# Performance work log

Measured on AMD Instinct MI355X. Metric: run time of the kernel, lower is better.

## Reference

```python
import jax, jax.numpy as jnp
import numpy as np

SIZE = 4096
LOG_N = 12  # log2(SIZE)
BATCH = 8192


def setup_inputs() -> dict:
    key = jax.random.key(0)
    k1, k2 = jax.random.split(key)
    x = jax.random.normal(k1, (BATCH, SIZE), dtype=jnp.float32)
    # one (SIZE//2, 2, 2) real twiddle bank per layer, stacked; init ~ randn/sqrt(2)
    twiddles = jax.random.normal(k2, (LOG_N, SIZE // 2, 2, 2), dtype=jnp.float32) / np.sqrt(2.0).astype(np.float32)
    return {"x": x, "twiddles": twiddles}


def _butterfly_forward(x, twiddles):
    # x: [B, n]; twiddles: [log_n, n//2, 2, 2]
    B, n = x.shape
    log_n = twiddles.shape[0]
    out = x
    for layer in range(log_n):
        stride = 2 ** (log_n - layer - 1)
        n_blocks = n // (2 * stride)
        # block b, offset i: top = out[:, b, 0, i], bot = out[:, b, 1, i]
        xr = out.reshape(B, n_blocks, 2, stride)
        top = xr[:, :, 0, :]  # [B, nb, stride]
        bot = xr[:, :, 1, :]
        # twiddle_idx = b*stride + i  ->  reshape to (nb, stride, 2, 2)
        w = twiddles[layer].reshape(n_blocks, stride, 2, 2)
        new_top = w[None, :, :, 0, 0] * top + w[None, :, :, 0, 1] * bot
        new_bot = w[None, :, :, 1, 0] * top + w[None, :, :, 1, 1] * bot
        out = jnp.stack([new_top, new_bot], axis=2).reshape(B, n)
    return out


def reference(x, twiddles):
    return _butterfly_forward(x, twiddles)
```

## Files before the change

kernel.cpp:

```cpp
#include <hip/hip_runtime.h>

#define ROWS 4
#define N 4096
#define BATCH 8192
#define S_AB 264
#define HALF 5248
#define S_BC 328
#define NWS_F4 (8 * 2048)

typedef float v4f __attribute__((ext_vector_type(4)));

__device__ __forceinline__ void layer_compute(float (&v)[ROWS][16],
                                              const float4 (&w)[8],
                                              const int bit) {
    const int d = 1 << bit;
    #pragma unroll
    for (int pc = 0; pc < 8; ++pc) {
        const int lo = ((pc >> bit) << (bit + 1)) | (pc & (d - 1));
        const int hi = lo + d;
        #pragma unroll
        for (int r = 0; r < ROWS; ++r) {
            const float top = v[r][lo];
            const float bot = v[r][hi];
            v[r][lo] = w[pc].x * top + w[pc].y * bot;
            v[r][hi] = w[pc].z * top + w[pc].w * bot;
        }
    }
}

__global__ __launch_bounds__(256)
void permute_tw_kernel(const float* __restrict__ tw, float4* __restrict__ nws) {
    const int i = blockIdx.x * 256 + threadIdx.x;
    const int s  = i >> 11;
    const int j  = i & 2047;
    const int pc = j >> 8;
    const int a  = (j >> 4) & 15;
    const int cb = j & 15;
    const float4* tw4 = (const float4*)tw;
    const int src = (s < 4) ? (a * 128 + pc * 16 + cb)
                            : (a * 128 + cb * 8 + pc);
    nws[i] = tw4[(4 + s) * 2048 + src];
}

__global__ __launch_bounds__(256, 2)
void butterfly_kernel(const float* __restrict__ x,
                      const float* __restrict__ tw,
                      const float4* __restrict__ nws,
                      float* __restrict__ out) {
    __shared__ float lds[2 * HALF];
    float* bufA = lds;
    float* bufB = lds + HALF;
    const int t   = threadIdx.x;
    const int thi = t >> 4;
    const int tlo = t & 15;
    const int row0 = blockIdx.x * ROWS;

    const float4* tw4 = (const float4*)tw;

    float v[ROWS][16];

    #pragma unroll
    for (int r = 0; r < ROWS; ++r) {
        const float* xr = x + (size_t)(row0 + r) * N + t;
        #pragma unroll
        for (int a = 0; a < 16; ++a)
            v[r][a] = __builtin_nontemporal_load(xr + a * 256);
    }

    #pragma unroll
    for (int l = 0; l < 4; ++l) {
        float4 w[8];
        #pragma unroll
        for (int pc = 0; pc < 8; ++pc)
            w[pc] = tw4[l * 2048 + pc * 256 + t];
        layer_compute(v, w, 3 - l);
    }

    float4 wB[8];
    {
        #pragma unroll
        for (int a = 0; a < 16; ++a) bufA[a * S_AB + t] = v[0][a];
        #pragma unroll
        for (int a = 0; a < 16; ++a) bufB[a * S_AB + t] = v[1][a];
        #pragma unroll
        for (int pc = 0; pc < 8; ++pc)
            wB[pc] = nws[pc * 256 + t];
        __syncthreads();
        #pragma unroll
        for (int b = 0; b < 16; ++b) v[0][b] = bufA[thi * S_AB + b * 16 + tlo];
        #pragma unroll
        for (int b = 0; b < 16; ++b) v[1][b] = bufB[thi * S_AB + b * 16 + tlo];
        __syncthreads();
        #pragma unroll
        for (int a = 0; a < 16; ++a) bufA[a * S_AB + t] = v[2][a];
        #pragma unroll
        for (int a = 0; a < 16; ++a) bufB[a * S_AB + t] = v[3][a];
        __syncthreads();
        #pragma unroll
        for (int b = 0; b < 16; ++b) v[2][b] = bufA[thi * S_AB + b * 16 + tlo];
        #pragma unroll
        for (int b = 0; b < 16; ++b) v[3][b] = bufB[thi * S_AB + b * 16 + tlo];
    }

    layer_compute(v, wB, 3);
    #pragma unroll
    for (int l = 5; l < 8; ++l) {
        float4 w[8];
        #pragma unroll
        for (int pc = 0; pc < 8; ++pc)
            w[pc] = nws[(l - 4) * 2048 + pc * 256 + t];
        layer_compute(v, w, 3 - (l - 4));
    }

    float4 wC[8];
    {
        __syncthreads();
        #pragma unroll
        for (int b = 0; b < 16; ++b) bufA[thi * S_BC + b * 20 + tlo] = v[0][b];
        #pragma unroll
        for (int b = 0; b < 16; ++b) bufB[thi * S_BC + b * 20 + tlo] = v[1][b];
        #pragma unroll
        for (int pc = 0; pc < 8; ++pc)
            wC[pc] = nws[4 * 2048 + pc * 256 + t];
        __syncthreads();
        #pragma unroll
        for (int rr = 0; rr < 2; ++rr) {
            const float* bp = (rr ? bufB : bufA) + thi * S_BC + tlo * 20;
            #pragma unroll
            for (int q = 0; q < 4; ++q) {
                v4f c4 = *(const v4f*)(bp + 4 * q);
                v[rr][4 * q + 0] = c4.x; v[rr][4 * q + 1] = c4.y;
                v[rr][4 * q + 2] = c4.z; v[rr][4 * q + 3] = c4.w;
            }
        }
        __syncthreads();
        #pragma unroll
        for (int b = 0; b < 16; ++b) bufA[thi * S_BC + b * 20 + tlo] = v[2][b];
        #pragma unroll
        for (int b = 0; b < 16; ++b) bufB[thi * S_BC + b * 20 + tlo] = v[3][b];
        __syncthreads();
        #pragma unroll
        for (int rr = 2; rr < 4; ++rr) {
            const float* bp = (rr == 3 ? bufB : bufA) + thi * S_BC + tlo * 20;
            #pragma unroll
            for (int q = 0; q < 4; ++q) {
                v4f c4 = *(const v4f*)(bp + 4 * q);
                v[rr][4 * q + 0] = c4.x; v[rr][4 * q + 1] = c4.y;
                v[rr][4 * q + 2] = c4.z; v[rr][4 * q + 3] = c4.w;
            }
        }
    }

    layer_compute(v, wC, 3);
    #pragma unroll
    for (int l = 9; l < 12; ++l) {
        float4 w[8];
        #pragma unroll
        for (int pc = 0; pc < 8; ++pc)
            w[pc] = nws[(l - 4) * 2048 + pc * 256 + t];
        layer_compute(v, w, 3 - (l - 8));
    }

    {
        v4f* fA = (v4f*)bufA;
        v4f* fB = (v4f*)bufB;
        __syncthreads();
        #pragma unroll
        for (int h = 0; h < 2; ++h) {
            #pragma unroll
            for (int rr = 0; rr < 2; ++rr) {
                v4f* f = rr ? fB : fA;
                const int r = 2 * h + rr;
                #pragma unroll
                for (int q = 0; q < 4; ++q) {
                    v4f s4;
                    s4.x = v[r][4 * q + 0]; s4.y = v[r][4 * q + 1];
                    s4.z = v[r][4 * q + 2]; s4.w = v[r][4 * q + 3];
                    f[5 * t + q] = s4;
                }
            }
            __syncthreads();
            #pragma unroll
            for (int rr = 0; rr < 2; ++rr) {
                v4f* f = rr ? fB : fA;
                const int r = 2 * h + rr;
                float* orow = out + (size_t)(row0 + r) * N;
                #pragma unroll
                for (int k = 0; k < 4; ++k) {
                    const int m = k * 256 + t;
                    v4f s4 = f[m + (m >> 2)];
                    __builtin_nontemporal_store(s4, (v4f*)orow + m);
                }
            }
            if (h == 0) __syncthreads();
        }
    }
}

#define PAD_STRIDE 264
#define BUF_WORDS (16 * PAD_STRIDE)

__global__ __launch_bounds__(256, 3)
void butterfly_kernel_fb(const float* __restrict__ x,
                         const float* __restrict__ tw,
                         float* __restrict__ out) {
    __shared__ float lds[BUF_WORDS];
    const int t = threadIdx.x;
    const int thi = t >> 4, tlo = t & 15;
    const int row0 = blockIdx.x * 4;
    const float4* tw4 = (const float4*)tw;
    float v[4][16];
    #pragma unroll
    for (int r = 0; r < 4; ++r) {
        const float* xr = x + (size_t)(row0 + r) * N + t;
        #pragma unroll
        for (int a = 0; a < 16; ++a) v[r][a] = __builtin_nontemporal_load(xr + a * 256);
    }
    #pragma unroll
    for (int l = 0; l < 4; ++l) {
        float4 w[8];
        #pragma unroll
        for (int pc = 0; pc < 8; ++pc) w[pc] = tw4[l * 2048 + pc * 256 + t];
        layer_compute(v, w, 3 - l);
    }
    #pragma unroll
    for (int r = 0; r < 4; ++r) {
        #pragma unroll
        for (int a = 0; a < 16; ++a) lds[a * PAD_STRIDE + t] = v[r][a];
        __syncthreads();
        #pragma unroll
        for (int b = 0; b < 16; ++b) v[r][b] = lds[thi * PAD_STRIDE + b * 16 + tlo];
        __syncthreads();
    }
    #pragma unroll
    for (int l = 4; l < 8; ++l) {
        float4 w[8];
        #pragma unroll
        for (int pc = 0; pc < 8; ++pc) w[pc] = tw4[l * 2048 + thi * 128 + pc * 16 + tlo];
        layer_compute(v, w, 3 - (l - 4));
    }
    #pragma unroll
    for (int r = 0; r < 4; ++r) {
        #pragma unroll
        for (int b = 0; b < 16; ++b) lds[thi * PAD_STRIDE + b * 16 + tlo] = v[r][b];
        __syncthreads();
        const float* bp = &lds[thi * PAD_STRIDE + tlo * 16];
        #pragma unroll
        for (int q = 0; q < 4; ++q) {
            v4f c4 = *(const v4f*)(bp + 4 * q);
            v[r][4 * q + 0] = c4.x; v[r][4 * q + 1] = c4.y;
            v[r][4 * q + 2] = c4.z; v[r][4 * q + 3] = c4.w;
        }
        if (r != 3) __syncthreads();
    }
    #pragma unroll
    for (int l = 8; l < 12; ++l) {
        float4 w[8];
        #pragma unroll
        for (int pc = 0; pc < 8; ++pc) w[pc] = tw4[l * 2048 + thi * 128 + tlo * 8 + pc];
        layer_compute(v, w, 3 - (l - 8));
    }
    #pragma unroll
    for (int r = 0; r < 4; ++r) {
        float* orow = out + (size_t)(row0 + r) * N + 16 * t;
        #pragma unroll
        for (int q = 0; q < 4; ++q) {
            v4f s4;
            s4.x = v[r][4 * q + 0]; s4.y = v[r][4 * q + 1];
            s4.z = v[r][4 * q + 2]; s4.w = v[r][4 * q + 3];
            *(v4f*)(orow + 4 * q) = s4;
        }
    }
}

extern "C" void kernel_launch(void* const* d_in, const int* in_sizes, int n_in,
                              void* d_out, int out_size, void* d_ws, size_t ws_size,
                              hipStream_t stream) {
    const float* x  = (const float*)d_in[0];
    const float* tw = (const float*)d_in[1];
    float* out      = (float*)d_out;
    dim3 block(256);
    if (ws_size >= (size_t)NWS_F4 * 16u) {
        float4* nws = (float4*)d_ws;
        hipLaunchKernelGGL(permute_tw_kernel, dim3(64), block, 0, stream, tw, nws);
        hipLaunchKernelGGL(butterfly_kernel, dim3(BATCH / ROWS), block, 0, stream,
                           x, tw, nws, out);
    } else {
        hipLaunchKernelGGL(butterfly_kernel_fb, dim3(BATCH / 4), block, 0, stream,
                           x, tw, out);
    }
}
```

Measured before the change: 76.73 us.

## Shrink LDS with XOR swizzles, vectorize input loads, raise occupancy to three blocks

Replaces the padded LDS layouts (stride 328 and the 5-float output padding) with XOR-swizzled layouts, so both buffers fit in 2×4224 floats. This is meant to allow three blocks per CU instead of two. Input rows are now read with 128-bit loads and transposed through LDS instead of scalar strided nontemporal loads. The early twiddle prefetch overlapped with the LDS exchanges is dropped. This adds extra LDS round trips and barriers for the input, and tightens the register budget under the higher launch bound.

```diff
diff --git a/kernel.cpp b/kernel.cpp
--- a/kernel.cpp
+++ b/kernel.cpp
@@ -4,8 +4,7 @@
 #define N 4096
 #define BATCH 8192
 #define S_AB 264
-#define HALF 5248
-#define S_BC 328
+#define ARENA 4224
 #define NWS_F4 (8 * 2048)
 
 typedef float v4f __attribute__((ext_vector_type(4)));
@@ -42,29 +41,55 @@
     nws[i] = tw4[(4 + s) * 2048 + src];
 }
 
-__global__ __launch_bounds__(256, 2)
+__global__ __launch_bounds__(256, 3)
 void butterfly_kernel(const float* __restrict__ x,
                       const float* __restrict__ tw,
                       const float4* __restrict__ nws,
                       float* __restrict__ out) {
-    __shared__ float lds[2 * HALF];
+    __shared__ float lds[2 * ARENA];
     float* bufA = lds;
-    float* bufB = lds + HALF;
+    float* bufB = lds + ARENA;
     const int t   = threadIdx.x;
     const int thi = t >> 4;
     const int tlo = t & 15;
     const int row0 = blockIdx.x * ROWS;
-
     const float4* tw4 = (const float4*)tw;
 
     float v[ROWS][16];
 
-    #pragma unroll
-    for (int r = 0; r < ROWS; ++r) {
-        const float* xr = x + (size_t)(row0 + r) * N + t;
-        #pragma unroll
-        for (int a = 0; a < 16; ++a)
-            v[r][a] = __builtin_nontemporal_load(xr + a * 256);
+    {
+        const float* r0 = x + (size_t)(row0 + 0) * N + 4 * t;
+        const float* r1 = x + (size_t)(row0 + 1) * N + 4 * t;
+        const float* r2 = x + (size_t)(row0 + 2) * N + 4 * t;
+        const float* r3 = x + (size_t)(row0 + 3) * N + 4 * t;
+        v4f t0[4], t1[4];
+        #pragma unroll
+        for (int i = 0; i < 4; ++i) t0[i] = *(const v4f*)(r0 + i * 1024);
+        #pragma unroll
+        for (int i = 0; i < 4; ++i) t1[i] = *(const v4f*)(r1 + i * 1024);
+        #pragma unroll
+        for (int i = 0; i < 4; ++i) *(v4f*)(bufA + i * 1024 + 4 * t) = t0[i];
+        #pragma unroll
+        for (int i = 0; i < 4; ++i) *(v4f*)(bufB + i * 1024 + 4 * t) = t1[i];
+        #pragma unroll
+        for (int i = 0; i < 4; ++i) t0[i] = *(const v4f*)(r2 + i * 1024);
+        #pragma unroll
+        for (int i = 0; i < 4; ++i) t1[i] = *(const v4f*)(r3 + i * 1024);
+        __syncthreads();
+        #pragma unroll
+        for (int a = 0; a < 16; ++a) v[0][a] = bufA[a * 256 + t];
+        #pragma unroll
+        for (int a = 0; a < 16; ++a) v[1][a] = bufB[a * 256 + t];
+        __syncthreads();
+        #pragma unroll
+        for (int i = 0; i < 4; ++i) *(v4f*)(bufA + i * 1024 + 4 * t) = t0[i];
+        #pragma unroll
+        for (int i = 0; i < 4; ++i) *(v4f*)(bufB + i * 1024 + 4 * t) = t1[i];
+        __syncthreads();
+        #pragma unroll
+        for (int a = 0; a < 16; ++a) v[2][a] = bufA[a * 256 + t];
+        #pragma unroll
+        for (int a = 0; a < 16; ++a) v[3][a] = bufB[a * 256 + t];
     }
 
     #pragma unroll
@@ -76,35 +101,29 @@
         layer_compute(v, w, 3 - l);
     }
 
-    float4 wB[8];
-    {
-        #pragma unroll
-        for (int a = 0; a < 16; ++a) bufA[a * S_AB + t] = v[0][a];
-        #pragma unroll
-        for (int a = 0; a < 16; ++a) bufB[a * S_AB + t] = v[1][a];
-        #pragma unroll
-        for (int pc = 0; pc < 8; ++pc)
-            wB[pc] = nws[pc * 256 + t];
-        __syncthreads();
-        #pragma unroll
-        for (int b = 0; b < 16; ++b) v[0][b] = bufA[thi * S_AB + b * 16 + tlo];
-        #pragma unroll
-        for (int b = 0; b < 16; ++b) v[1][b] = bufB[thi * S_AB + b * 16 + tlo];
-        __syncthreads();
-        #pragma unroll
-        for (int a = 0; a < 16; ++a) bufA[a * S_AB + t] = v[2][a];
-        #pragma unroll
-        for (int a = 0; a < 16; ++a) bufB[a * S_AB + t] = v[3][a];
-        __syncthreads();
-        #pragma unroll
-        for (int b = 0; b < 16; ++b) v[2][b] = bufA[thi * S_AB + b * 16 + tlo];
-        #pragma unroll
-        for (int b = 0; b < 16; ++b) v[3][b] = bufB[thi * S_AB + b * 16 + tlo];
-    }
-
-    layer_compute(v, wB, 3);
-    #pragma unroll
-    for (int l = 5; l < 8; ++l) {
+    __syncthreads();
+    #pragma unroll
+    for (int a = 0; a < 16; ++a) bufA[a * S_AB + t] = v[0][a];
+    #pragma unroll
+    for (int a = 0; a < 16; ++a) bufB[a * S_AB + t] = v[1][a];
+    __syncthreads();
+    #pragma unroll
+    for (int b = 0; b < 16; ++b) v[0][b] = bufA[thi * S_AB + b * 16 + tlo];
+    #pragma unroll
+    for (int b = 0; b < 16; ++b) v[1][b] = bufB[thi * S_AB + b * 16 + tlo];
+    __syncthreads();
+    #pragma unroll
+    for (int a = 0; a < 16; ++a) bufA[a * S_AB + t] = v[2][a];
+    #pragma unroll
+    for (int a = 0; a < 16; ++a) bufB[a * S_AB + t] = v[3][a];
+    __syncthreads();
+    #pragma unroll
+    for (int b = 0; b < 16; ++b) v[2][b] = bufA[thi * S_AB + b * 16 + tlo];
+    #pragma unroll
+    for (int b = 0; b < 16; ++b) v[3][b] = bufB[thi * S_AB + b * 16 + tlo];
+
+    #pragma unroll
+    for (int l = 4; l < 8; ++l) {
         float4 w[8];
         #pragma unroll
         for (int pc = 0; pc < 8; ++pc)
@@ -112,48 +131,47 @@
         layer_compute(v, w, 3 - (l - 4));
     }
 
-    float4 wC[8];
     {
         __syncthreads();
         #pragma unroll
-        for (int b = 0; b < 16; ++b) bufA[thi * S_BC + b * 20 + tlo] = v[0][b];
-        #pragma unroll
-        for (int b = 0; b < 16; ++b) bufB[thi * S_BC + b * 20 + tlo] = v[1][b];
-        #pragma unroll
-        for (int pc = 0; pc < 8; ++pc)
-            wC[pc] = nws[4 * 2048 + pc * 256 + t];
+        for (int b = 0; b < 16; ++b) {
+            const int coff = 4 * (((tlo >> 2) ^ (b & 3))) + (tlo & 3);
+            bufA[thi * S_AB + b * 16 + coff] = v[0][b];
+            bufB[thi * S_AB + b * 16 + coff] = v[1][b];
+        }
         __syncthreads();
         #pragma unroll
         for (int rr = 0; rr < 2; ++rr) {
-            const float* bp = (rr ? bufB : bufA) + thi * S_BC + tlo * 20;
+            const float* bp = (rr ? bufB : bufA) + thi * S_AB + tlo * 16;
             #pragma unroll
             for (int q = 0; q < 4; ++q) {
-                v4f c4 = *(const v4f*)(bp + 4 * q);
+                v4f c4 = *(const v4f*)(bp + 4 * (q ^ (tlo & 3)));
                 v[rr][4 * q + 0] = c4.x; v[rr][4 * q + 1] = c4.y;
                 v[rr][4 * q + 2] = c4.z; v[rr][4 * q + 3] = c4.w;
             }
         }
         __syncthreads();
         #pragma unroll
-        for (int b = 0; b < 16; ++b) bufA[thi * S_BC + b * 20 + tlo] = v[2][b];
-        #pragma unroll
-        for (int b = 0; b < 16; ++b) bufB[thi * S_BC + b * 20 + tlo] = v[3][b];
+        for (int b = 0; b < 16; ++b) {
+            const int coff = 4 * (((tlo >> 2) ^ (b & 3))) + (tlo & 3);
+            bufA[thi * S_AB + b * 16 + coff] = v[2][b];
+            bufB[thi * S_AB + b * 16 + coff] = v[3][b];
+        }
         __syncthreads();
         #pragma unroll
         for (int rr = 2; rr < 4; ++rr) {
-            const float* bp = (rr == 3 ? bufB : bufA) + thi * S_BC + tlo * 20;
+            const float* bp = (rr == 3 ? bufB : bufA) + thi * S_AB + tlo * 16;
             #pragma unroll
             for (int q = 0; q < 4; ++q) {
-                v4f c4 = *(const v4f*)(bp + 4 * q);
+                v4f c4 = *(const v4f*)(bp + 4 * (q ^ (tlo & 3)));
                 v[rr][4 * q + 0] = c4.x; v[rr][4 * q + 1] = c4.y;
                 v[rr][4 * q + 2] = c4.z; v[rr][4 * q + 3] = c4.w;
             }
         }
     }
 
-    layer_compute(v, wC, 3);
-    #pragma unroll
-    for (int l = 9; l < 12; ++l) {
+    #pragma unroll
+    for (int l = 8; l < 12; ++l) {
         float4 w[8];
         #pragma unroll
         for (int pc = 0; pc < 8; ++pc)
@@ -164,6 +182,7 @@
     {
         v4f* fA = (v4f*)bufA;
         v4f* fB = (v4f*)bufB;
+        const int wsel = (t >> 2) & 3;
         __syncthreads();
         #pragma unroll
         for (int h = 0; h < 2; ++h) {
@@ -176,7 +195,7 @@
                     v4f s4;
                     s4.x = v[r][4 * q + 0]; s4.y = v[r][4 * q + 1];
                     s4.z = v[r][4 * q + 2]; s4.w = v[r][4 * q + 3];
-                    f[5 * t + q] = s4;
+                    f[4 * t + (q ^ wsel)] = s4;
                 }
             }
             __syncthreads();
@@ -187,9 +206,9 @@
                 float* orow = out + (size_t)(row0 + r) * N;
                 #pragma unroll
                 for (int k = 0; k < 4; ++k) {
-                    const int m = k * 256 + t;
-                    v4f s4 = f[m + (m >> 2)];
-                    __builtin_nontemporal_store(s4, (v4f*)orow + m);
+                    const int j = k * 256 + t;
+                    v4f s4 = f[(j & ~3) | ((j & 3) ^ ((j >> 4) & 3))];
+                    __builtin_nontemporal_store(s4, (v4f*)orow + j);
                 }
             }
             if (h == 0) __syncthreads();
```

Measured after the change: 66.71 us. 13.1% less time.
